# Performance work log

Hardware: AMD Instinct MI355X
Metric: run time of the kernel (lower is better)

Reference implementation:

```python
import jax, jax.numpy as jnp
import numpy as np

TOP_K = 2
NUM_EXPERTS = 64
SEQ, BS, HS = 2048, 4, 4096
TOKENS = SEQ * BS  # tokens_per_batch
TOL = 1e-4
EPS = 1e-8


def sinkhorn(temp_cost):
    # temp_cost: (T, E) float32 logits. Mirrors SinkhornRouter.sinkhorn exactly.
    cost = jnp.exp(temp_cost)
    n0, n1 = cost.shape
    # initial d0 (overwritten inside loop in torch too, kept for fidelity of carry dtype/shape)
    d0 = (TOKENS / NUM_EXPERTS) * jnp.sum(jnp.exp(2.0 * temp_cost), axis=1)
    d1 = jnp.ones((n1,), dtype=cost.dtype)
    err0 = jnp.asarray(1e9, dtype=cost.dtype)

    def cond(carry):
        _, _, err = carry
        return err > TOL

    def body(carry):
        d0, d1, _ = carry  # d1 here plays the role of d1_old
        d0_new = (1.0 / n0) / (jnp.sum(d1 * cost, axis=1) + EPS)          # (T,)
        d1_new = (1.0 / n1) / (jnp.sum(d0_new[:, None] * cost, axis=0) + EPS)  # (E,)
        err = jnp.mean(jnp.abs(d1 - d1_new))
        return (d0_new, d1_new, err)

    d0, d1, _ = jax.lax.while_loop(cond, body, (d0, d1, err0))
    return d1 * cost * d0[:, None]


def setup_inputs() -> dict:
    key = jax.random.key(0)
    kx, kw = jax.random.split(key)
    x = jax.random.normal(kx, (SEQ, BS, HS), dtype=jnp.float32)
    W = jax.random.normal(kw, (NUM_EXPERTS, HS), dtype=jnp.float32) * 0.02
    return {"x": x, "W": W}


def reference(x, W):
    # router logits: (T, E)
    logits = jnp.reshape(x, (-1, x.shape[-1])) @ W.T
    # Sinkhorn normalization is done in fp32 under no_grad in torch -> stop_gradient
    norm_logits = sinkhorn(jax.lax.stop_gradient(logits).astype(jnp.float32))
    _, indices = jax.lax.top_k(norm_logits, TOP_K)  # (T, top_k) int32
    # top_k > 1 -> softmax activation (fp32, cast back)
    probs = jax.nn.softmax(logits.astype(jnp.float32), axis=-1).astype(logits.dtype)
    scores = jnp.take_along_axis(probs, indices, axis=1)  # (T, top_k)
    return scores, indices
```

## Files before the change

### kernel.cpp

```cpp
#include <hip/hip_runtime.h>
#include <hip/hip_cooperative_groups.h>
#include <math.h>

namespace cg = cooperative_groups;

namespace {
constexpr int kTokens = 8192;
constexpr int kHS = 4096;
constexpr float kTol = 1e-4f;
constexpr float kEps = 1e-8f;
constexpr int kMaxIters = 1000;
constexpr int kSinkBlocks = 64;
constexpr size_t kTagFloats = 128;
constexpr size_t kGdataFloats = 2 * 64 * 64;
constexpr size_t kPartOff = kTagFloats + kGdataFloats;
constexpr size_t kSliceFloats = (size_t)kTokens * 64;
constexpr size_t kWtpFloats = (size_t)(kHS / 4) * 64 * 4;
}

__device__ __forceinline__ float wave_sum(float v) {
#pragma unroll
  for (int o = 32; o; o >>= 1) v += __shfl_xor(v, o, 64);
  return v;
}

__global__ void __launch_bounds__(128, 2)
k_logits(const float* __restrict__ X, const float* __restrict__ W,
         float* __restrict__ part, int KS) {
  __shared__ float xs[32][132];
  __shared__ float wsh[32][68];
  const int tid = threadIdx.x;
  const int tx = tid & 7;
  const int ty = tid >> 3;
  const int tb = blockIdx.x & 63;
  const int s = blockIdx.x >> 6;
  const int t0 = tb * 128;
  const int k0 = s * KS;
  const int cx = tid & 7;
  const int rx = tid >> 3;

  const float* xsrc = X + (size_t)(t0 + rx) * kHS + k0 + 4 * cx;
  const float* wsrc = W + (size_t)rx * kHS + k0 + 4 * cx;

  float acc[8][8];
#pragma unroll
  for (int i = 0; i < 8; ++i)
#pragma unroll
    for (int j = 0; j < 8; ++j) acc[i][j] = 0.0f;

  const int nkt = KS / 32;
  float4 xa[8], wa[4];
#pragma unroll
  for (int p = 0; p < 8; ++p)
    xa[p] = *(const float4*)(xsrc + (size_t)p * 16 * kHS);
#pragma unroll
  for (int p = 0; p < 4; ++p)
    wa[p] = *(const float4*)(wsrc + (size_t)p * 16 * kHS);

  for (int kt = 0; kt < nkt; ++kt) {
    __syncthreads();
#pragma unroll
    for (int p = 0; p < 8; ++p) {
      xs[4 * cx + 0][rx + 16 * p] = xa[p].x;
      xs[4 * cx + 1][rx + 16 * p] = xa[p].y;
      xs[4 * cx + 2][rx + 16 * p] = xa[p].z;
      xs[4 * cx + 3][rx + 16 * p] = xa[p].w;
    }
#pragma unroll
    for (int p = 0; p < 4; ++p) {
      wsh[4 * cx + 0][rx + 16 * p] = wa[p].x;
      wsh[4 * cx + 1][rx + 16 * p] = wa[p].y;
      wsh[4 * cx + 2][rx + 16 * p] = wa[p].z;
      wsh[4 * cx + 3][rx + 16 * p] = wa[p].w;
    }
    __syncthreads();
    if (kt + 1 < nkt) {
      const int ko = (kt + 1) * 32;
#pragma unroll
      for (int p = 0; p < 8; ++p)
        xa[p] = *(const float4*)(xsrc + (size_t)p * 16 * kHS + ko);
#pragma unroll
      for (int p = 0; p < 4; ++p)
        wa[p] = *(const float4*)(wsrc + (size_t)p * 16 * kHS + ko);
    }
#pragma unroll 8
    for (int k = 0; k < 32; ++k) {
      const float4 x0 = *(const float4*)&xs[k][8 * ty];
      const float4 x1 = *(const float4*)&xs[k][8 * ty + 4];
      const float4 w0 = *(const float4*)&wsh[k][8 * tx];
      const float4 w1 = *(const float4*)&wsh[k][8 * tx + 4];
      const float xr[8] = {x0.x, x0.y, x0.z, x0.w, x1.x, x1.y, x1.z, x1.w};
      const float wr[8] = {w0.x, w0.y, w0.z, w0.w, w1.x, w1.y, w1.z, w1.w};
#pragma unroll
      for (int i = 0; i < 8; ++i)
#pragma unroll
        for (int j = 0; j < 8; ++j) acc[i][j] = fmaf(xr[i], wr[j], acc[i][j]);
    }
  }

  float* pb = part + ((size_t)s * kTokens + t0 + 8 * ty) * 64 + 8 * tx;
#pragma unroll
  for (int i = 0; i < 8; ++i) {
    *(float4*)(pb + (size_t)i * 64) =
        make_float4(acc[i][0], acc[i][1], acc[i][2], acc[i][3]);
    *(float4*)(pb + (size_t)i * 64 + 4) =
        make_float4(acc[i][4], acc[i][5], acc[i][6], acc[i][7]);
  }
}

__global__ void __launch_bounds__(1024, 1)
k_sinkhorn(const float* __restrict__ part, int S, float* __restrict__ out,
           unsigned* __restrict__ tags, float* __restrict__ gdata) {
  const int tid = threadIdx.x;
  const int lane = tid & 63;
  const int wid = __builtin_amdgcn_readfirstlane(tid >> 6);
  const int blk = blockIdx.x;
  __shared__ float lds[1024];

  const int t0 = blk * 128 + wid * 8;
  float lg[8], cst[8];
#pragma unroll
  for (int t = 0; t < 8; ++t) {
    float a = 0.0f;
    for (int s = 0; s < S; ++s)
      a += part[((size_t)s * kTokens + t0 + t) * 64 + lane];
    lg[t] = a;
    cst[t] = expf(a);
  }

  float d1 = 1.0f;
  float d0v[8];
  int buf = 0;
  for (int it = 0; it < kMaxIters; ++it) {
    float p = 0.0f;
#pragma unroll
    for (int t = 0; t < 8; ++t) {
      const float s = wave_sum(d1 * cst[t]);
      const float d0t = (1.0f / 8192.0f) / (s + kEps);
      d0v[t] = d0t;
      p = fmaf(d0t, cst[t], p);
    }
    __syncthreads();
    lds[wid * 64 + lane] = p;
    __syncthreads();
    const unsigned want = (unsigned)(it + 1);
    if (wid == 0) {
      float bp = 0.0f;
#pragma unroll
      for (int w = 0; w < 16; ++w) bp += lds[w * 64 + lane];
      __hip_atomic_store(&gdata[((size_t)buf * 64 + blk) * 64 + lane], bp,
                         __ATOMIC_RELAXED, __HIP_MEMORY_SCOPE_AGENT);
      __threadfence();
      if (lane == 0)
        __hip_atomic_store(&tags[buf * 64 + blk], want, __ATOMIC_RELEASE,
                           __HIP_MEMORY_SCOPE_AGENT);
      while (__hip_atomic_load(&tags[buf * 64 + lane], __ATOMIC_ACQUIRE,
                               __HIP_MEMORY_SCOPE_AGENT) != want) {
        __builtin_amdgcn_s_sleep(1);
      }
    }
    __syncthreads();
    float s2 = 0.0f;
#pragma unroll
    for (int i = 0; i < 4; ++i)
      s2 += __hip_atomic_load(
          &gdata[((size_t)buf * 64 + wid * 4 + i) * 64 + lane],
          __ATOMIC_RELAXED, __HIP_MEMORY_SCOPE_AGENT);
    lds[wid * 64 + lane] = s2;
    __syncthreads();
    float colsum = 0.0f;
#pragma unroll
    for (int w = 0; w < 16; ++w) colsum += lds[w * 64 + lane];
    const float d1n = (1.0f / 64.0f) / (colsum + kEps);
    const float err = wave_sum(fabsf(d1 - d1n)) * (1.0f / 64.0f);
    d1 = d1n;
    buf ^= 1;
    if (err <= kTol) break;
  }

#pragma unroll
  for (int t = 0; t < 8; ++t) {
    const float lgv = lg[t];
    float m = lgv;
#pragma unroll
    for (int o = 32; o; o >>= 1) m = fmaxf(m, __shfl_xor(m, o, 64));
    const float ex = expf(lgv - m);
    const float den = wave_sum(ex);
    const float prob = ex / den;

    const float v = (d1 * cst[t]) * d0v[t];
    float v1 = v;
    int i1 = lane;
#pragma unroll
    for (int o = 32; o; o >>= 1) {
      const float ov = __shfl_xor(v1, o, 64);
      const int oi = __shfl_xor(i1, o, 64);
      if (ov > v1 || (ov == v1 && oi < i1)) { v1 = ov; i1 = oi; }
    }
    float v2 = (lane == i1) ? -INFINITY : v;
    int i2 = lane;
#pragma unroll
    for (int o = 32; o; o >>= 1) {
      const float ov = __shfl_xor(v2, o, 64);
      const int oi = __shfl_xor(i2, o, 64);
      if (ov > v2 || (ov == v2 && oi < i2)) { v2 = ov; i2 = oi; }
    }
    const float p1 = __shfl(prob, i1, 64);
    const float p2 = __shfl(prob, i2, 64);
    if (lane == 0) {
      const int row = t0 + t;
      out[row * 2 + 0] = p1;
      out[row * 2 + 1] = p2;
      out[2 * kTokens + row * 2 + 0] = (float)i1;
      out[2 * kTokens + row * 2 + 1] = (float)i2;
    }
  }
}

__global__ void __launch_bounds__(256, 1)
sinkhorn_router(const float* __restrict__ X, const float* __restrict__ W,
                float* __restrict__ out, float* __restrict__ ws) {
  cg::grid_group grid = cg::this_grid();
  const int tid = threadIdx.x;
  const int lane = tid & 63;
  const int wid = __builtin_amdgcn_readfirstlane(tid >> 6);
  const int blk = blockIdx.x;

  float4* wtp = reinterpret_cast<float4*>(ws);
  float* gpart = ws + kWtpFloats;
  __shared__ float lds[256];

  {
    const int j = blk * 256 + tid;
    const int e = j & 63;
    const int k4 = j >> 6;
    wtp[j] = *reinterpret_cast<const float4*>(W + (size_t)e * kHS + 4 * (size_t)k4);
  }
  grid.sync();

  const int t0 = blk * 32 + wid * 8;
  const float* xb = X + (size_t)t0 * kHS;
  float lg[8];
#pragma unroll
  for (int t = 0; t < 8; ++t) lg[t] = 0.0f;

#pragma unroll 2
  for (int k4 = 0; k4 < kHS / 4; ++k4) {
    const float4 w = wtp[k4 * 64 + lane];
#pragma unroll
    for (int t = 0; t < 8; ++t) {
      const float* xr = xb + (size_t)t * kHS + 4 * (size_t)k4;
      float a = lg[t];
      a = fmaf(xr[0], w.x, a);
      a = fmaf(xr[1], w.y, a);
      a = fmaf(xr[2], w.z, a);
      a = fmaf(xr[3], w.w, a);
      lg[t] = a;
    }
  }

  float cst[8];
#pragma unroll
  for (int t = 0; t < 8; ++t) cst[t] = expf(lg[t]);

  float d1 = 1.0f;
  float d0v[8];
  int buf = 0;
  for (int it = 0; it < kMaxIters; ++it) {
    float p = 0.0f;
#pragma unroll
    for (int t = 0; t < 8; ++t) {
      const float s = wave_sum(d1 * cst[t]);
      const float d0t = (1.0f / 8192.0f) / (s + kEps);
      d0v[t] = d0t;
      p = fmaf(d0t, cst[t], p);
    }
    __syncthreads();
    lds[wid * 64 + lane] = p;
    __syncthreads();
    if (wid == 0) {
      const float bp =
          lds[lane] + lds[64 + lane] + lds[128 + lane] + lds[192 + lane];
      gpart[buf * (256 * 64) + blk * 64 + lane] = bp;
    }
    grid.sync();
    const float* gp = gpart + buf * (256 * 64);
    float s = 0.0f;
#pragma unroll 8
    for (int b = 0; b < 64; ++b) s += gp[(wid * 64 + b) * 64 + lane];
    lds[wid * 64 + lane] = s;
    __syncthreads();
    const float colsum =
        lds[lane] + lds[64 + lane] + lds[128 + lane] + lds[192 + lane];
    const float d1n = (1.0f / 64.0f) / (colsum + kEps);
    const float err = wave_sum(fabsf(d1 - d1n)) * (1.0f / 64.0f);
    d1 = d1n;
    buf ^= 1;
    if (err <= kTol) break;
  }

#pragma unroll
  for (int t = 0; t < 8; ++t) {
    const float lgv = lg[t];
    float m = lgv;
#pragma unroll
    for (int o = 32; o; o >>= 1) m = fmaxf(m, __shfl_xor(m, o, 64));
    const float ex = expf(lgv - m);
    const float den = wave_sum(ex);
    const float prob = ex / den;

    const float v = (d1 * cst[t]) * d0v[t];
    float v1 = v;
    int i1 = lane;
#pragma unroll
    for (int o = 32; o; o >>= 1) {
      const float ov = __shfl_xor(v1, o, 64);
      const int oi = __shfl_xor(i1, o, 64);
      if (ov > v1 || (ov == v1 && oi < i1)) { v1 = ov; i1 = oi; }
    }
    float v2 = (lane == i1) ? -INFINITY : v;
    int i2 = lane;
#pragma unroll
    for (int o = 32; o; o >>= 1) {
      const float ov = __shfl_xor(v2, o, 64);
      const int oi = __shfl_xor(i2, o, 64);
      if (ov > v2 || (ov == v2 && oi < i2)) { v2 = ov; i2 = oi; }
    }
    const float p1 = __shfl(prob, i1, 64);
    const float p2 = __shfl(prob, i2, 64);
    if (lane == 0) {
      const int row = t0 + t;
      out[row * 2 + 0] = p1;
      out[row * 2 + 1] = p2;
      out[2 * kTokens + row * 2 + 0] = (float)i1;
      out[2 * kTokens + row * 2 + 1] = (float)i2;
    }
  }
}

extern "C" void kernel_launch(void* const* d_in, const int* in_sizes, int n_in,
                              void* d_out, int out_size, void* d_ws,
                              size_t ws_size, hipStream_t stream) {
  const float* X = (const float*)d_in[0];
  const float* W = (const float*)d_in[1];
  float* out = (float*)d_out;
  float* ws = (float*)d_ws;

  int S = 0;
  for (int cand : {16, 8, 4, 2, 1}) {
    const size_t need = (kPartOff + (size_t)cand * kSliceFloats) * 4;
    if (need <= ws_size) { S = cand; break; }
  }

  if (S == 0) {
    void* args[] = {(void*)&X, (void*)&W, (void*)&out, (void*)&ws};
    hipLaunchCooperativeKernel((const void*)sinkhorn_router, dim3(256),
                               dim3(256), args, 0, stream);
    return;
  }

  unsigned* tags = reinterpret_cast<unsigned*>(ws);
  float* gdata = ws + kTagFloats;
  float* part = ws + kPartOff;

  const int KS = kHS / S;
  hipLaunchKernelGGL(k_logits, dim3(64 * S), dim3(128), 0, stream, X, W, part,
                     KS);
  hipLaunchKernelGGL(k_sinkhorn, dim3(kSinkBlocks), dim3(1024), 0, stream,
                     part, S, out, tags, gdata);
}
```

Baseline: 279.3 us.

## Load X tiles directly from global memory instead of staging through LDS

The logits GEMM kernel no longer stages the X tile in shared memory. Each thread now reads its 8 token rows straight from global memory as float4 vectors, while only W stays in LDS. The aim is to cut LDS traffic, transposed stores and shared-memory footprint. In exchange, the 8 threads that share a token row (same ty, different tx) each load the same X data, which leans on L1/L2 for reuse and drops the register prefetch of X.

```diff
diff --git a/kernel.cpp b/kernel.cpp
--- a/kernel.cpp
+++ b/kernel.cpp
@@ -27,7 +27,6 @@
 __global__ void __launch_bounds__(128, 2)
 k_logits(const float* __restrict__ X, const float* __restrict__ W,
          float* __restrict__ part, int KS) {
-  __shared__ float xs[32][132];
   __shared__ float wsh[32][68];
   const int tid = threadIdx.x;
   const int tx = tid & 7;
@@ -36,11 +35,12 @@
   const int s = blockIdx.x >> 6;
   const int t0 = tb * 128;
   const int k0 = s * KS;
-  const int cx = tid & 7;
-  const int rx = tid >> 3;
-
-  const float* xsrc = X + (size_t)(t0 + rx) * kHS + k0 + 4 * cx;
-  const float* wsrc = W + (size_t)rx * kHS + k0 + 4 * cx;
+
+  const int wr = tid & 63;
+  const int wc0 = (tid >> 6) * 4;
+
+  const float* xbase = X + (size_t)(t0 + 8 * ty) * kHS + k0;
+  const float* wbase = W + (size_t)wr * kHS + k0;
 
   float acc[8][8];
 #pragma unroll
@@ -49,52 +49,51 @@
     for (int j = 0; j < 8; ++j) acc[i][j] = 0.0f;
 
   const int nkt = KS / 32;
-  float4 xa[8], wa[4];
-#pragma unroll
-  for (int p = 0; p < 8; ++p)
-    xa[p] = *(const float4*)(xsrc + (size_t)p * 16 * kHS);
+  float4 wpre[4];
 #pragma unroll
   for (int p = 0; p < 4; ++p)
-    wa[p] = *(const float4*)(wsrc + (size_t)p * 16 * kHS);
+    wpre[p] = *(const float4*)(wbase + 4 * (wc0 + p));
 
   for (int kt = 0; kt < nkt; ++kt) {
     __syncthreads();
 #pragma unroll
-    for (int p = 0; p < 8; ++p) {
-      xs[4 * cx + 0][rx + 16 * p] = xa[p].x;
-      xs[4 * cx + 1][rx + 16 * p] = xa[p].y;
-      xs[4 * cx + 2][rx + 16 * p] = xa[p].z;
-      xs[4 * cx + 3][rx + 16 * p] = xa[p].w;
-    }
-#pragma unroll
     for (int p = 0; p < 4; ++p) {
-      wsh[4 * cx + 0][rx + 16 * p] = wa[p].x;
-      wsh[4 * cx + 1][rx + 16 * p] = wa[p].y;
-      wsh[4 * cx + 2][rx + 16 * p] = wa[p].z;
-      wsh[4 * cx + 3][rx + 16 * p] = wa[p].w;
+      const int c = wc0 + p;
+      wsh[4 * c + 0][wr] = wpre[p].x;
+      wsh[4 * c + 1][wr] = wpre[p].y;
+      wsh[4 * c + 2][wr] = wpre[p].z;
+      wsh[4 * c + 3][wr] = wpre[p].w;
     }
     __syncthreads();
     if (kt + 1 < nkt) {
-      const int ko = (kt + 1) * 32;
-#pragma unroll
-      for (int p = 0; p < 8; ++p)
-        xa[p] = *(const float4*)(xsrc + (size_t)p * 16 * kHS + ko);
+      const int ko = 32 * (kt + 1);
 #pragma unroll
       for (int p = 0; p < 4; ++p)
-        wa[p] = *(const float4*)(wsrc + (size_t)p * 16 * kHS + ko);
-    }
-#pragma unroll 8
-    for (int k = 0; k < 32; ++k) {
-      const float4 x0 = *(const float4*)&xs[k][8 * ty];
-      const float4 x1 = *(const float4*)&xs[k][8 * ty + 4];
-      const float4 w0 = *(const float4*)&wsh[k][8 * tx];
-      const float4 w1 = *(const float4*)&wsh[k][8 * tx + 4];
-      const float xr[8] = {x0.x, x0.y, x0.z, x0.w, x1.x, x1.y, x1.z, x1.w};
-      const float wr[8] = {w0.x, w0.y, w0.z, w0.w, w1.x, w1.y, w1.z, w1.w};
+        wpre[p] = *(const float4*)(wbase + ko + 4 * (wc0 + p));
+    }
+    const int kk0 = kt * 32;
+#pragma unroll 2
+    for (int kb = 0; kb < 8; ++kb) {
+      float4 xq[8];
 #pragma unroll
       for (int i = 0; i < 8; ++i)
-#pragma unroll
-        for (int j = 0; j < 8; ++j) acc[i][j] = fmaf(xr[i], wr[j], acc[i][j]);
+        xq[i] = *(const float4*)(xbase + (size_t)i * kHS + kk0 + 4 * kb);
+#pragma unroll
+      for (int u = 0; u < 4; ++u) {
+        const float4 w0 = *(const float4*)&wsh[4 * kb + u][8 * tx];
+        const float4 w1 = *(const float4*)&wsh[4 * kb + u][8 * tx + 4];
+        const float wr8[8] = {w0.x, w0.y, w0.z, w0.w, w1.x, w1.y, w1.z, w1.w};
+#pragma unroll
+        for (int i = 0; i < 8; ++i) {
+          const float xv = (u == 0)   ? xq[i].x
+                           : (u == 1) ? xq[i].y
+                           : (u == 2) ? xq[i].z
+                                      : xq[i].w;
+#pragma unroll
+          for (int j = 0; j < 8; ++j)
+            acc[i][j] = fmaf(xv, wr8[j], acc[i][j]);
+        }
+      }
     }
   }
 
```

Result: slower. 298.4 us (+6.9%).
